# Performance work log

Hardware: AMD Instinct MI355X
Metric: run time of the kernel (lower is better)

## Reference

```python
import jax, jax.numpy as jnp
import numpy as np

B, L, D_MODEL = 2, 2048, 1024
HEADS, DH, K = 8, 128, 64  # d_head = d_model // heads, kernel_width window
DILATIONS = np.array([1, 1, 2, 2, 4, 4, 8, 8], dtype=np.int32)  # per-head dilation


def setup_inputs() -> dict:
    key = jax.random.key(0)
    ks = jax.random.split(key, 8)
    s_in = 1.0 / np.sqrt(D_MODEL)       # kaiming-uniform-ish fan_in bound
    s_c = 1.0 / np.sqrt(HEADS * DH)
    return {
        "query": jax.random.normal(ks[0], (B, L, D_MODEL), dtype=jnp.float32),
        "key": jax.random.normal(ks[1], (B, L, D_MODEL), dtype=jnp.float32),
        "value": jax.random.normal(ks[2], (B, L, D_MODEL), dtype=jnp.float32),
        "Wq": jax.random.uniform(ks[3], (HEADS, DH, D_MODEL), minval=-s_in, maxval=s_in),
        "bq": jnp.zeros((HEADS, DH), dtype=jnp.float32),
        "Wk": jax.random.uniform(ks[4], (HEADS, DH, D_MODEL), minval=-s_in, maxval=s_in),
        "bk": jnp.zeros((HEADS, DH), dtype=jnp.float32),
        "Wv": jax.random.uniform(ks[5], (HEADS, DH, D_MODEL), minval=-s_in, maxval=s_in),
        "bv": jnp.zeros((HEADS, DH), dtype=jnp.float32),
        "Wc": jax.random.uniform(ks[6], (D_MODEL, HEADS * DH), minval=-s_c, maxval=s_c),
        "bc": jnp.zeros((D_MODEL,), dtype=jnp.float32),
    }


def reference(query, key, value, Wq, bq, Wk, bk, Wv, bv, Wc, bc):
    Lq = query.shape[-2]
    # per-head linear projections: [B,L,D] x [H,DH,D] -> [B,H,L,DH]
    q = jnp.einsum('bld,hed->bhle', query, Wq) + bq[:, None, :]
    k = jnp.einsum('bld,hed->bhle', key, Wk) + bk[:, None, :]
    v = jnp.einsum('bld,hed->bhle', value, Wv) + bv[:, None, :]

    # dilated, centered local windows (per-head dilation)
    offsets = jnp.arange(K) - (K - 1) // 2                     # [K]
    dil = jnp.asarray(DILATIONS)                               # [H]
    idx = (jnp.arange(Lq)[None, :, None]
           + offsets[None, None, :] * dil[:, None, None])      # [H, L, K]
    valid = (idx >= 0) & (idx < Lq)
    idxc = jnp.clip(idx, 0, Lq - 1)

    # gather per-head windows: x [B,H,L,DH], idx [H,L,K] -> [B,H,L,K,DH]
    gather = jax.vmap(lambda xh, ih: xh[:, ih], in_axes=(1, 0), out_axes=1)
    k_win = gather(k, idxc)
    v_win = gather(v, idxc)

    # banded attention (original applies no 1/sqrt(d) scaling)
    scores = jnp.einsum('bhld,bhlkd->bhlk', q, k_win)
    scores = jnp.where(valid[None], scores, jnp.asarray(-1e9, scores.dtype))
    attn = jax.nn.softmax(scores, axis=-1)
    out = jnp.einsum('bhlk,bhlkd->bhld', attn, v_win)

    # merge heads and collapse back to d_model
    out = out.transpose(0, 2, 1, 3).reshape(out.shape[0], Lq, HEADS * DH)
    return out @ Wc.T + bc
```

## Files before the change

kernel.cpp:

```cpp
#include <hip/hip_runtime.h>
#include <hip/hip_bf16.h>
#include <stdint.h>

#define NB 2
#define LQ 2048
#define DMODEL 1024
#define NH 8
#define DH 128
#define KWIN 64

typedef __attribute__((ext_vector_type(8))) short short8;
typedef __attribute__((ext_vector_type(4))) float f32x4;

#define AS1 __attribute__((address_space(1)))
#define AS3 __attribute__((address_space(3)))

__device__ __forceinline__ ushort f2bf(float f) {
  uint u = __float_as_uint(f);
  return (ushort)((u + 0x7fffu + ((u >> 16) & 1u)) >> 16);
}
__device__ __forceinline__ float bflo(uint u) { return __uint_as_float(u << 16); }
__device__ __forceinline__ float bfhi(uint u) { return __uint_as_float(u & 0xffff0000u); }

__global__ void cvt_all(const float4* __restrict__ q, const float4* __restrict__ k,
                        const float4* __restrict__ v, const float4* __restrict__ wq,
                        const float4* __restrict__ wk, const float4* __restrict__ wv,
                        const float4* __restrict__ wc, ushort4* __restrict__ dst) {
  const int n4in = (NB * LQ * DMODEL) / 4;
  const int n4w = (NH * DH * DMODEL) / 4;
  const int total = 3 * n4in + 4 * n4w;
  const int stride = gridDim.x * blockDim.x;
  for (int i = blockIdx.x * blockDim.x + threadIdx.x; i < total; i += stride) {
    const float4* src;
    int off;
    if (i < 3 * n4in) {
      const int r = i >> 20;
      off = i & (n4in - 1);
      src = (r == 0) ? q : ((r == 1) ? k : v);
    } else {
      const int j = i - 3 * n4in;
      const int r = j >> 18;
      off = j & (n4w - 1);
      src = (r == 0) ? wq : ((r == 1) ? wk : ((r == 2) ? wv : wc));
    }
    float4 x = src[off];
    dst[i] = make_ushort4(f2bf(x.x), f2bf(x.y), f2bf(x.z), f2bf(x.w));
  }
}

__global__ __launch_bounds__(512, 2) void gemm256p(
    const ushort* __restrict__ A0, const ushort* __restrict__ B0,
    const float* __restrict__ c0, ushort* __restrict__ D0,
    const ushort* __restrict__ A1, const ushort* __restrict__ B1,
    const float* __restrict__ c1, ushort* __restrict__ D1,
    const ushort* __restrict__ A2, const ushort* __restrict__ B2,
    const float* __restrict__ c2, ushort* __restrict__ D2,
    int M, int N, int Kd) {
  const int gx = gridDim.x, gy = gridDim.y;
  const int nblk = gx * gy * gridDim.z;
  const int fid = (blockIdx.z * gy + blockIdx.y) * gx + blockIdx.x;
  const int cpx = nblk >> 3;
  const int nid = (fid & 7) * cpx + (fid >> 3);
  const int z = nid / (gx * gy);
  const int rem = nid % (gx * gy);
  const int m0 = (rem / gx) * 256;
  const int n0 = (rem % gx) * 256;

  const ushort* A = (z == 0) ? A0 : ((z == 1) ? A1 : A2);
  const ushort* Bt = (z == 0) ? B0 : ((z == 1) ? B1 : B2);
  const float* bias = (z == 0) ? c0 : ((z == 1) ? c1 : c2);
  ushort* Cv = (z == 0) ? D0 : ((z == 1) ? D1 : D2);

  __shared__ ushort LDS[4][16384];

  const int tid = threadIdx.x;
  const int wave = tid >> 6, lane = tid & 63;
  const int wm = wave >> 2, wn = wave & 3;
  const int lrow = lane & 15, kgrp = lane >> 4;

  const ushort* gsrc[4];
  int lofs[4];
#pragma unroll
  for (int qq = 0; qq < 4; ++qq) {
    const int half = qq & 1;
    const int o = half * 8192 + tid * 16;
    const int pr = o >> 7;
    const int s = (o >> 4) & 7;
    const int x = s ^ (pr & 7);
    const int row = 2 * pr + (x & 1);
    const int chunk = (x >> 1) * 8;
    lofs[qq] = (qq >> 1) * 8192 + half * 4096 + tid * 8;
    gsrc[qq] = (qq < 2) ? (A + (size_t)(m0 + row) * Kd + chunk)
                        : (Bt + (size_t)(n0 + row) * Kd + chunk);
  }

  auto STAGE2 = [&](int tt, int p) {
    ushort* sl = &LDS[tt & 3][0];
    const int kt = tt << 5;
    __builtin_amdgcn_global_load_lds((const AS1 void*)(gsrc[p] + kt),
                                     (AS3 void*)(sl + lofs[p]), 16, 0, 0);
    __builtin_amdgcn_global_load_lds((const AS1 void*)(gsrc[2 + p] + kt),
                                     (AS3 void*)(sl + lofs[2 + p]), 16, 0, 0);
  };

  int aoff[8], boff[4];
#pragma unroll
  for (int mi = 0; mi < 8; ++mi) {
    const int r = wm * 128 + mi * 16 + lrow;
    aoff[mi] = (r >> 1) * 64 + ((((kgrp << 1) | (r & 1)) ^ ((r >> 1) & 7)) * 8);
  }
#pragma unroll
  for (int ni = 0; ni < 4; ++ni) {
    const int r = wn * 64 + ni * 16 + lrow;
    boff[ni] = 8192 + (r >> 1) * 64 + ((((kgrp << 1) | (r & 1)) ^ ((r >> 1) & 7)) * 8);
  }

  f32x4 acc[8][4] = {};
  const int NT = Kd >> 5;

  STAGE2(0, 0); STAGE2(0, 1);
  STAGE2(1, 0); STAGE2(1, 1);

  for (int t = 0; t < NT; ++t) {
    const ushort* sl = &LDS[t & 3][0];
    if (t < NT - 2) {
      STAGE2(t + 2, 0);
      asm volatile("s_waitcnt vmcnt(6)" ::: "memory");
    } else if (t == NT - 2) {
      asm volatile("s_waitcnt vmcnt(4)" ::: "memory");
    } else {
      asm volatile("s_waitcnt vmcnt(0)" ::: "memory");
    }
    __builtin_amdgcn_sched_barrier(0);
    __builtin_amdgcn_s_barrier();
    __builtin_amdgcn_sched_barrier(0);

    short8 af[8], bfr[4];
#pragma unroll
    for (int m = 0; m < 4; ++m) af[m] = *(const short8*)(sl + aoff[m]);
#pragma unroll
    for (int n = 0; n < 4; ++n) bfr[n] = *(const short8*)(sl + boff[n]);
    asm volatile("s_waitcnt lgkmcnt(0)" ::: "memory");
    __builtin_amdgcn_sched_barrier(0);
    __builtin_amdgcn_s_setprio(1);
#pragma unroll
    for (int m = 0; m < 4; ++m)
#pragma unroll
      for (int n = 0; n < 4; ++n)
        acc[m][n] = __builtin_amdgcn_mfma_f32_16x16x32_bf16(af[m], bfr[n], acc[m][n], 0, 0, 0);
    __builtin_amdgcn_s_setprio(0);
    __builtin_amdgcn_sched_barrier(0);

    if (t < NT - 2) STAGE2(t + 2, 1);
#pragma unroll
    for (int m = 4; m < 8; ++m) af[m] = *(const short8*)(sl + aoff[m]);
    asm volatile("s_waitcnt lgkmcnt(0)" ::: "memory");
    __builtin_amdgcn_sched_barrier(0);
    __builtin_amdgcn_s_setprio(1);
#pragma unroll
    for (int m = 4; m < 8; ++m)
#pragma unroll
      for (int n = 0; n < 4; ++n)
        acc[m][n] = __builtin_amdgcn_mfma_f32_16x16x32_bf16(af[m], bfr[n], acc[m][n], 0, 0, 0);
    __builtin_amdgcn_s_setprio(0);
    __builtin_amdgcn_sched_barrier(0);
  }

  const int cbase = n0 + wn * 64;
  const int rbase = m0 + wm * 128;
  float bv[4];
#pragma unroll
  for (int n = 0; n < 4; ++n) bv[n] = bias[cbase + n * 16 + lrow];

#pragma unroll
  for (int m = 0; m < 8; ++m) {
#pragma unroll
    for (int n = 0; n < 4; ++n) {
      const int col = cbase + n * 16 + lrow;
#pragma unroll
      for (int j = 0; j < 4; ++j) {
        const int row = rbase + m * 16 + kgrp * 4 + j;
        Cv[(size_t)row * N + col] = f2bf(acc[m][n][j] + bv[n]);
      }
    }
  }
}

__global__ __launch_bounds__(256, 4) void gemm_out(
    const ushort* __restrict__ A, const ushort* __restrict__ Bt,
    const float* __restrict__ bias, float* __restrict__ Cv, int M, int N, int Kd) {
  const int gx = gridDim.x, gy = gridDim.y;
  const int nblk = gx * gy;
  const int fid = blockIdx.y * gx + blockIdx.x;
  const int cpx = nblk >> 3;
  const int nid = (fid & 7) * cpx + (fid >> 3);
  const int m0 = (nid / gx) * 128;
  const int n0 = (nid % gx) * 128;

  __shared__ ushort As[2][128 * 32];
  __shared__ ushort Bs[2][128 * 32];

  const int tid = threadIdx.x;
  const int wave = tid >> 6, lane = tid & 63;
  const int wm = wave >> 1, wn = wave & 1;
  const int lrow = lane & 15, kgrp = lane >> 4;

  const int b0 = tid * 16;
  const int b1 = b0 + 4096;
  const int r0 = b0 >> 6, cc0 = (b0 & 63) >> 1;
  const int r1 = b1 >> 6, cc1 = (b1 & 63) >> 1;

  const ushort* gA0 = A + (size_t)(m0 + r0) * Kd + cc0;
  const ushort* gA1 = A + (size_t)(m0 + r1) * Kd + cc1;
  const ushort* gB0 = Bt + (size_t)(n0 + r0) * Kd + cc0;
  const ushort* gB1 = Bt + (size_t)(n0 + r1) * Kd + cc1;

  auto stage = [&](int buf, int kt) {
    __builtin_amdgcn_global_load_lds((const AS1 void*)(gA0 + kt),
                                     (AS3 void*)(As[buf] + (b0 >> 1)), 16, 0, 0);
    __builtin_amdgcn_global_load_lds((const AS1 void*)(gA1 + kt),
                                     (AS3 void*)(As[buf] + (b1 >> 1)), 16, 0, 0);
    __builtin_amdgcn_global_load_lds((const AS1 void*)(gB0 + kt),
                                     (AS3 void*)(Bs[buf] + (b0 >> 1)), 16, 0, 0);
    __builtin_amdgcn_global_load_lds((const AS1 void*)(gB1 + kt),
                                     (AS3 void*)(Bs[buf] + (b1 >> 1)), 16, 0, 0);
  };

  f32x4 acc[4][4] = {};

  auto compute = [&](int buf) {
    short8 af[4], bfr[4];
#pragma unroll
    for (int m = 0; m < 4; ++m)
      af[m] = *(const short8*)(As[buf] + (wm * 64 + m * 16 + lrow) * 32 + kgrp * 8);
#pragma unroll
    for (int n = 0; n < 4; ++n)
      bfr[n] = *(const short8*)(Bs[buf] + (wn * 64 + n * 16 + lrow) * 32 + kgrp * 8);
#pragma unroll
    for (int m = 0; m < 4; ++m)
#pragma unroll
      for (int n = 0; n < 4; ++n)
        acc[m][n] = __builtin_amdgcn_mfma_f32_16x16x32_bf16(af[m], bfr[n], acc[m][n], 0, 0, 0);
  };

  const int nt = Kd >> 5;
  stage(0, 0);
  __syncthreads();
  int cur = 0;
  for (int it = 0; it < nt - 1; ++it) {
    stage(cur ^ 1, (it + 1) << 5);
    compute(cur);
    __syncthreads();
    cur ^= 1;
  }
  compute(cur);

  const int cbase = n0 + wn * 64;
  const int rbase = m0 + wm * 64;
  float bv[4];
#pragma unroll
  for (int n = 0; n < 4; ++n) bv[n] = bias[cbase + n * 16 + lrow];

#pragma unroll
  for (int m = 0; m < 4; ++m) {
#pragma unroll
    for (int n = 0; n < 4; ++n) {
      const int col = cbase + n * 16 + lrow;
#pragma unroll
      for (int j = 0; j < 4; ++j) {
        const int row = rbase + m * 16 + kgrp * 4 + j;
        Cv[(size_t)row * N + col] = acc[m][n][j] + bv[n];
      }
    }
  }
}

__global__ __launch_bounds__(128) void banded_attn_mfma(
    const ushort* __restrict__ qp, const ushort* __restrict__ kp,
    const ushort* __restrict__ vp, ushort* __restrict__ ao) {
  __shared__ ushort Qs[32 * 128];
  __shared__ ushort Ks[96 * 128];
  __shared__ ushort Vs[112 * 128];
  __shared__ ushort Ps[2][16 * 104];
  __shared__ ushort Os[2][16 * 128];

  const int tid = threadIdx.x;
  const int wv = tid >> 6;
  const int lane = tid & 63;
  const int lrow = lane & 15, kgrp = lane >> 4;

  const int blk = blockIdx.x;
  const int chunk = blk & 63;
  const int h = (blk >> 6) & 7;
  const int b = blk >> 9;
  const int sh = h >> 1;
  const int dil = 1 << sh;
  const int Ld = LQ >> sh;
  const int rres = chunk >> (6 - sh);
  const int tile = chunk & ((64 >> sh) - 1);
  const int t0 = tile << 5;
  const int p0 = t0 - 32;

  const size_t headoff = (size_t)h * DH;
  const size_t bbase = (size_t)b * LQ * (NH * DH);

  const int srow = lane >> 4;
  const int sc = lane & 15;
  for (int it = wv; it < 60; it += 2) {
    int rbase, pstart;
    const ushort* g;
    ushort* ld;
    if (it < 8) {
      rbase = it * 4; pstart = t0; g = qp; ld = Qs;
    } else if (it < 32) {
      rbase = (it - 8) * 4; pstart = p0; g = kp; ld = Ks;
    } else {
      rbase = (it - 32) * 4; pstart = p0; g = vp; ld = Vs;
    }
    int row = rbase + srow;
    int key = (row ^ (row >> 3)) & 7;
    int cs = sc ^ key;
    int t = pstart + row;
    t = t < 0 ? 0 : (t >= Ld ? Ld - 1 : t);
    int l = rres + t * dil;
    const ushort* src = g + bbase + (size_t)l * (NH * DH) + headoff + cs * 8;
    __builtin_amdgcn_global_load_lds((const AS1 void*)src,
                                     (AS3 void*)(ld + rbase * 128), 16, 0, 0);
  }
  __syncthreads();

  const int iblk = wv << 4;
  f32x4 accs[5] = {};
#pragma unroll
  for (int ks = 0; ks < 4; ++ks) {
    const int qrow = iblk + lrow;
    const int qslot = (ks * 4 + kgrp) ^ ((qrow ^ (qrow >> 3)) & 7);
    short8 qf = *(const short8*)(Qs + qrow * 128 + qslot * 8);
#pragma unroll
    for (int t = 0; t < 5; ++t) {
      const int krow = (wv + t) * 16 + lrow;
      const int kslot = (ks * 4 + kgrp) ^ ((krow ^ (krow >> 3)) & 7);
      short8 kf = *(const short8*)(Ks + krow * 128 + kslot * 8);
      accs[t] = __builtin_amdgcn_mfma_f32_16x16x32_bf16(qf, kf, accs[t], 0, 0, 0);
    }
  }

  float dens[4];
#pragma unroll
  for (int j = 0; j < 4; ++j) {
    const int i_b = iblk + kgrp * 4 + j;
    float mj = -1e30f;
#pragma unroll
    for (int t = 0; t < 5; ++t) {
      const int jj = (wv + t) * 16 + lrow;
      const int p = p0 + jj;
      const bool ok = (jj >= i_b + 1) && (jj <= i_b + 64) && (p >= 0) && (p < Ld);
      float v = ok ? accs[t][j] : -1e30f;
      accs[t][j] = v;
      mj = fmaxf(mj, v);
    }
#pragma unroll
    for (int off = 1; off < 16; off <<= 1) mj = fmaxf(mj, __shfl_xor(mj, off));
    float dj = 0.f;
#pragma unroll
    for (int t = 0; t < 5; ++t) {
      float e = __expf(accs[t][j] - mj);
      accs[t][j] = e;
      dj += e;
    }
#pragma unroll
    for (int off = 1; off < 16; off <<= 1) dj += __shfl_xor(dj, off);
    dens[j] = dj;
  }

  ushort* Pw = Ps[wv];
#pragma unroll
  for (int j = 0; j < 4; ++j) {
    const int prow = kgrp * 4 + j;
#pragma unroll
    for (int t = 0; t < 5; ++t) Pw[prow * 104 + t * 16 + lrow] = f2bf(accs[t][j]);
    Pw[prow * 104 + 80 + lrow] = 0;
  }

  f32x4 accv[8] = {};
#pragma unroll
  for (int ks = 0; ks < 3; ++ks) {
    short8 pf = *(const short8*)(Pw + lrow * 104 + ks * 32 + kgrp * 8);
#pragma unroll
    for (int dt = 0; dt < 8; ++dt) {
      short8 vf;
#pragma unroll
      for (int rr = 0; rr < 8; ++rr) {
        const int vrow = iblk + ks * 32 + kgrp * 8 + rr;
        const int d = dt * 16 + lrow;
        const int slot = (d >> 3) ^ ((vrow ^ (vrow >> 3)) & 7);
        vf[rr] = (short)Vs[vrow * 128 + slot * 8 + (d & 7)];
      }
      accv[dt] = __builtin_amdgcn_mfma_f32_16x16x32_bf16(pf, vf, accv[dt], 0, 0, 0);
    }
  }

  ushort* Ow = Os[wv];
#pragma unroll
  for (int j = 0; j < 4; ++j) {
    const float inv = 1.f / dens[j];
    const int orow = kgrp * 4 + j;
#pragma unroll
    for (int dt = 0; dt < 8; ++dt)
      Ow[orow * 128 + dt * 16 + lrow] = f2bf(accv[dt][j] * inv);
  }
#pragma unroll
  for (int pass = 0; pass < 4; ++pass) {
    const int i_loc = pass * 4 + srow;
    const int tq = t0 + iblk + i_loc;
    const int l = rres + tq * dil;
    short8 vvv = *(const short8*)(Ow + i_loc * 128 + sc * 8);
    *(short8*)(ao + bbase + (size_t)l * (NH * DH) + headoff + sc * 8) = vvv;
  }
}

extern "C" void kernel_launch(void* const* d_in, const int* in_sizes, int n_in,
                              void* d_out, int out_size, void* d_ws, size_t ws_size,
                              hipStream_t stream) {
  const float* q = (const float*)d_in[0];
  const float* k = (const float*)d_in[1];
  const float* v = (const float*)d_in[2];
  const float* Wq = (const float*)d_in[3];
  const float* bq = (const float*)d_in[4];
  const float* Wk = (const float*)d_in[5];
  const float* bk = (const float*)d_in[6];
  const float* Wv = (const float*)d_in[7];
  const float* bv = (const float*)d_in[8];
  const float* Wc = (const float*)d_in[9];
  const float* bc = (const float*)d_in[10];

  const size_t NIN = (size_t)NB * LQ * DMODEL;
  const size_t NW = (size_t)NH * DH * DMODEL;

  ushort* qin = (ushort*)d_ws;
  ushort* kin = qin + NIN;
  ushort* vin = kin + NIN;
  ushort* wqb = vin + NIN;
  ushort* wkb = wqb + NW;
  ushort* wvb = wkb + NW;
  ushort* wcb = wvb + NW;
  ushort* qp = wcb + NW;
  ushort* kp = qp + NIN;
  ushort* vp = kp + NIN;
  ushort* aob = vp + NIN;

  hipLaunchKernelGGL(cvt_all, dim3(2048), dim3(256), 0, stream,
                     (const float4*)q, (const float4*)k, (const float4*)v,
                     (const float4*)Wq, (const float4*)Wk, (const float4*)Wv,
                     (const float4*)Wc, (ushort4*)qin);

  dim3 g1(DMODEL / 256, (NB * LQ) / 256, 3);
  hipLaunchKernelGGL(gemm256p, g1, dim3(512), 0, stream,
                     qin, wqb, bq, qp,
                     kin, wkb, bk, kp,
                     vin, wvb, bv, vp,
                     NB * LQ, DMODEL, DMODEL);

  hipLaunchKernelGGL(banded_attn_mfma, dim3(NB * NH * 64), dim3(128), 0, stream,
                     qp, kp, vp, aob);

  dim3 g2(DMODEL / 128, (NB * LQ) / 128);
  hipLaunchKernelGGL(gemm_out, g2, dim3(256), 0, stream,
                     aob, wcb, bc, (float*)d_out, NB * LQ, DMODEL, DMODEL);
}
```

Measured before the change: 99.81 us.

## Fuse fp32-to-bf16 activation conversion into QKV projection GEMM loads

The separate conversion pass over the q/k/v activations is removed. The QKV GEMM now loads fp32 A tiles into registers, converts them to bf16 and writes them to LDS, while B tiles still go through direct global-to-LDS loads. The pipeline is reworked into a register-staged, three-deep prefetch with an unswizzled LDS layout, and the weight-only conversion kernel is simplified. This removes a full write and re-read of the bf16 activations. In exchange the GEMM reads twice as many A bytes, uses more registers, and the unswizzled LDS layout may cause bank conflicts.

```diff
diff --git a/kernel.cpp b/kernel.cpp
--- a/kernel.cpp
+++ b/kernel.cpp
@@ -22,38 +22,26 @@
 __device__ __forceinline__ float bflo(uint u) { return __uint_as_float(u << 16); }
 __device__ __forceinline__ float bfhi(uint u) { return __uint_as_float(u & 0xffff0000u); }
 
-__global__ void cvt_all(const float4* __restrict__ q, const float4* __restrict__ k,
-                        const float4* __restrict__ v, const float4* __restrict__ wq,
-                        const float4* __restrict__ wk, const float4* __restrict__ wv,
-                        const float4* __restrict__ wc, ushort4* __restrict__ dst) {
-  const int n4in = (NB * LQ * DMODEL) / 4;
-  const int n4w = (NH * DH * DMODEL) / 4;
-  const int total = 3 * n4in + 4 * n4w;
-  const int stride = gridDim.x * blockDim.x;
-  for (int i = blockIdx.x * blockDim.x + threadIdx.x; i < total; i += stride) {
-    const float4* src;
-    int off;
-    if (i < 3 * n4in) {
-      const int r = i >> 20;
-      off = i & (n4in - 1);
-      src = (r == 0) ? q : ((r == 1) ? k : v);
-    } else {
-      const int j = i - 3 * n4in;
-      const int r = j >> 18;
-      off = j & (n4w - 1);
-      src = (r == 0) ? wq : ((r == 1) ? wk : ((r == 2) ? wv : wc));
-    }
-    float4 x = src[off];
-    dst[i] = make_ushort4(f2bf(x.x), f2bf(x.y), f2bf(x.z), f2bf(x.w));
-  }
-}
-
-__global__ __launch_bounds__(512, 2) void gemm256p(
-    const ushort* __restrict__ A0, const ushort* __restrict__ B0,
+__global__ void cvt_w(const float4* __restrict__ a, const float4* __restrict__ b,
+                      const float4* __restrict__ c, const float4* __restrict__ d,
+                      ushort* __restrict__ da, ushort* __restrict__ db,
+                      ushort* __restrict__ dc, ushort* __restrict__ dd, int n4) {
+  int stride = gridDim.x * blockDim.x;
+  for (int i = blockIdx.x * blockDim.x + threadIdx.x; i < n4; i += stride) {
+    float4 x = a[i], y = b[i], z = c[i], w = d[i];
+    *(ushort4*)(da + 4 * (size_t)i) = make_ushort4(f2bf(x.x), f2bf(x.y), f2bf(x.z), f2bf(x.w));
+    *(ushort4*)(db + 4 * (size_t)i) = make_ushort4(f2bf(y.x), f2bf(y.y), f2bf(y.z), f2bf(y.w));
+    *(ushort4*)(dc + 4 * (size_t)i) = make_ushort4(f2bf(z.x), f2bf(z.y), f2bf(z.z), f2bf(z.w));
+    *(ushort4*)(dd + 4 * (size_t)i) = make_ushort4(f2bf(w.x), f2bf(w.y), f2bf(w.z), f2bf(w.w));
+  }
+}
+
+__global__ __launch_bounds__(512, 2) void gemm256f(
+    const float* __restrict__ A0f, const ushort* __restrict__ B0,
     const float* __restrict__ c0, ushort* __restrict__ D0,
-    const ushort* __restrict__ A1, const ushort* __restrict__ B1,
+    const float* __restrict__ A1f, const ushort* __restrict__ B1,
     const float* __restrict__ c1, ushort* __restrict__ D1,
-    const ushort* __restrict__ A2, const ushort* __restrict__ B2,
+    const float* __restrict__ A2f, const ushort* __restrict__ B2,
     const float* __restrict__ c2, ushort* __restrict__ D2,
     int M, int N, int Kd) {
   const int gx = gridDim.x, gy = gridDim.y;
@@ -66,7 +54,7 @@
   const int m0 = (rem / gx) * 256;
   const int n0 = (rem % gx) * 256;
 
-  const ushort* A = (z == 0) ? A0 : ((z == 1) ? A1 : A2);
+  const float* Af = (z == 0) ? A0f : ((z == 1) ? A1f : A2f);
   const ushort* Bt = (z == 0) ? B0 : ((z == 1) ? B1 : B2);
   const float* bias = (z == 0) ? c0 : ((z == 1) ? c1 : c2);
   ushort* Cv = (z == 0) ? D0 : ((z == 1) ? D1 : D2);
@@ -78,92 +66,103 @@
   const int wm = wave >> 2, wn = wave & 3;
   const int lrow = lane & 15, kgrp = lane >> 4;
 
-  const ushort* gsrc[4];
-  int lofs[4];
-#pragma unroll
-  for (int qq = 0; qq < 4; ++qq) {
-    const int half = qq & 1;
-    const int o = half * 8192 + tid * 16;
-    const int pr = o >> 7;
-    const int s = (o >> 4) & 7;
-    const int x = s ^ (pr & 7);
-    const int row = 2 * pr + (x & 1);
-    const int chunk = (x >> 1) * 8;
-    lofs[qq] = (qq >> 1) * 8192 + half * 4096 + tid * 8;
-    gsrc[qq] = (qq < 2) ? (A + (size_t)(m0 + row) * Kd + chunk)
-                        : (Bt + (size_t)(n0 + row) * Kd + chunk);
-  }
-
-  auto STAGE2 = [&](int tt, int p) {
+  const int ac0 = wave * 128 + lane;
+  const int ac1 = ac0 + 64;
+  const float* gA0 = Af + (size_t)(m0 + (ac0 >> 2)) * Kd + (ac0 & 3) * 8;
+  const float* gA1 = Af + (size_t)(m0 + (ac1 >> 2)) * Kd + (ac1 & 3) * 8;
+
+  const int o0 = tid * 16;
+  const int o1 = o0 + 8192;
+  const ushort* gB0 = Bt + (size_t)(n0 + (o0 >> 6)) * Kd + ((o0 & 63) >> 1);
+  const ushort* gB1 = Bt + (size_t)(n0 + (o1 >> 6)) * Kd + ((o1 & 63) >> 1);
+
+  float4 fa0[4], fa1[4];
+
+  auto AISSUE = [&](int tt, float4* d) {
+    const float* s0 = gA0 + (tt << 5);
+    const float* s1 = gA1 + (tt << 5);
+    d[0] = *(const float4*)(s0);
+    d[1] = *(const float4*)(s0 + 4);
+    d[2] = *(const float4*)(s1);
+    d[3] = *(const float4*)(s1 + 4);
+  };
+  auto BISSUE = [&](int tt) {
     ushort* sl = &LDS[tt & 3][0];
-    const int kt = tt << 5;
-    __builtin_amdgcn_global_load_lds((const AS1 void*)(gsrc[p] + kt),
-                                     (AS3 void*)(sl + lofs[p]), 16, 0, 0);
-    __builtin_amdgcn_global_load_lds((const AS1 void*)(gsrc[2 + p] + kt),
-                                     (AS3 void*)(sl + lofs[2 + p]), 16, 0, 0);
+    __builtin_amdgcn_global_load_lds((const AS1 void*)(gB0 + (tt << 5)),
+                                     (AS3 void*)(sl + 8192 + (o0 >> 1)), 16, 0, 0);
+    __builtin_amdgcn_global_load_lds((const AS1 void*)(gB1 + (tt << 5)),
+                                     (AS3 void*)(sl + 8192 + (o1 >> 1)), 16, 0, 0);
+  };
+  auto AWRITE = [&](int tt, const float4* d) {
+    ushort* sl = &LDS[tt & 3][0];
+    short8 w0, w1;
+    w0[0] = (short)f2bf(d[0].x); w0[1] = (short)f2bf(d[0].y);
+    w0[2] = (short)f2bf(d[0].z); w0[3] = (short)f2bf(d[0].w);
+    w0[4] = (short)f2bf(d[1].x); w0[5] = (short)f2bf(d[1].y);
+    w0[6] = (short)f2bf(d[1].z); w0[7] = (short)f2bf(d[1].w);
+    w1[0] = (short)f2bf(d[2].x); w1[1] = (short)f2bf(d[2].y);
+    w1[2] = (short)f2bf(d[2].z); w1[3] = (short)f2bf(d[2].w);
+    w1[4] = (short)f2bf(d[3].x); w1[5] = (short)f2bf(d[3].y);
+    w1[6] = (short)f2bf(d[3].z); w1[7] = (short)f2bf(d[3].w);
+    *(short8*)(sl + ac0 * 8) = w0;
+    *(short8*)(sl + ac1 * 8) = w1;
   };
 
   int aoff[8], boff[4];
 #pragma unroll
-  for (int mi = 0; mi < 8; ++mi) {
-    const int r = wm * 128 + mi * 16 + lrow;
-    aoff[mi] = (r >> 1) * 64 + ((((kgrp << 1) | (r & 1)) ^ ((r >> 1) & 7)) * 8);
-  }
-#pragma unroll
-  for (int ni = 0; ni < 4; ++ni) {
-    const int r = wn * 64 + ni * 16 + lrow;
-    boff[ni] = 8192 + (r >> 1) * 64 + ((((kgrp << 1) | (r & 1)) ^ ((r >> 1) & 7)) * 8);
-  }
+  for (int mi = 0; mi < 8; ++mi) aoff[mi] = (wm * 128 + mi * 16 + lrow) * 32 + kgrp * 8;
+#pragma unroll
+  for (int ni = 0; ni < 4; ++ni) boff[ni] = 8192 + (wn * 64 + ni * 16 + lrow) * 32 + kgrp * 8;
 
   f32x4 acc[8][4] = {};
   const int NT = Kd >> 5;
 
-  STAGE2(0, 0); STAGE2(0, 1);
-  STAGE2(1, 0); STAGE2(1, 1);
-
-  for (int t = 0; t < NT; ++t) {
+  AISSUE(0, fa0); BISSUE(0);
+  AISSUE(1, fa1); BISSUE(1);
+  asm volatile("s_waitcnt vmcnt(6)" ::: "memory");
+  __builtin_amdgcn_sched_barrier(0);
+  AWRITE(0, fa0);
+  AISSUE(2, fa0); BISSUE(2);
+  asm volatile("s_waitcnt lgkmcnt(0)" ::: "memory");
+  __builtin_amdgcn_sched_barrier(0);
+  __builtin_amdgcn_s_barrier();
+
+  auto BODY = [&](int t, float4* S) {
+    if (t < NT - 1) {
+      if (t < NT - 2) {
+        asm volatile("s_waitcnt vmcnt(6)" ::: "memory");
+      } else {
+        asm volatile("s_waitcnt vmcnt(0)" ::: "memory");
+      }
+      __builtin_amdgcn_sched_barrier(0);
+      AWRITE(t + 1, S);
+    }
+    if (t + 3 < NT) { AISSUE(t + 3, S); BISSUE(t + 3); }
+
     const ushort* sl = &LDS[t & 3][0];
-    if (t < NT - 2) {
-      STAGE2(t + 2, 0);
-      asm volatile("s_waitcnt vmcnt(6)" ::: "memory");
-    } else if (t == NT - 2) {
-      asm volatile("s_waitcnt vmcnt(4)" ::: "memory");
-    } else {
-      asm volatile("s_waitcnt vmcnt(0)" ::: "memory");
-    }
+    short8 af[8], bfr[4];
+#pragma unroll
+    for (int m = 0; m < 8; ++m) af[m] = *(const short8*)(sl + aoff[m]);
+#pragma unroll
+    for (int n = 0; n < 4; ++n) bfr[n] = *(const short8*)(sl + boff[n]);
+    asm volatile("s_waitcnt lgkmcnt(0)" ::: "memory");
     __builtin_amdgcn_sched_barrier(0);
     __builtin_amdgcn_s_barrier();
     __builtin_amdgcn_sched_barrier(0);
 
-    short8 af[8], bfr[4];
-#pragma unroll
-    for (int m = 0; m < 4; ++m) af[m] = *(const short8*)(sl + aoff[m]);
-#pragma unroll
-    for (int n = 0; n < 4; ++n) bfr[n] = *(const short8*)(sl + boff[n]);
-    asm volatile("s_waitcnt lgkmcnt(0)" ::: "memory");
-    __builtin_amdgcn_sched_barrier(0);
     __builtin_amdgcn_s_setprio(1);
 #pragma unroll
-    for (int m = 0; m < 4; ++m)
+    for (int m = 0; m < 8; ++m)
 #pragma unroll
       for (int n = 0; n < 4; ++n)
         acc[m][n] = __builtin_amdgcn_mfma_f32_16x16x32_bf16(af[m], bfr[n], acc[m][n], 0, 0, 0);
     __builtin_amdgcn_s_setprio(0);
     __builtin_amdgcn_sched_barrier(0);
-
-    if (t < NT - 2) STAGE2(t + 2, 1);
-#pragma unroll
-    for (int m = 4; m < 8; ++m) af[m] = *(const short8*)(sl + aoff[m]);
-    asm volatile("s_waitcnt lgkmcnt(0)" ::: "memory");
-    __builtin_amdgcn_sched_barrier(0);
-    __builtin_amdgcn_s_setprio(1);
-#pragma unroll
-    for (int m = 4; m < 8; ++m)
-#pragma unroll
-      for (int n = 0; n < 4; ++n)
-        acc[m][n] = __builtin_amdgcn_mfma_f32_16x16x32_bf16(af[m], bfr[n], acc[m][n], 0, 0, 0);
-    __builtin_amdgcn_s_setprio(0);
-    __builtin_amdgcn_sched_barrier(0);
+  };
+
+  for (int t = 0; t < NT; t += 2) {
+    BODY(t, fa1);
+    BODY(t + 1, fa0);
   }
 
   const int cbase = n0 + wn * 64;
@@ -437,10 +436,7 @@
   const size_t NIN = (size_t)NB * LQ * DMODEL;
   const size_t NW = (size_t)NH * DH * DMODEL;
 
-  ushort* qin = (ushort*)d_ws;
-  ushort* kin = qin + NIN;
-  ushort* vin = kin + NIN;
-  ushort* wqb = vin + NIN;
+  ushort* wqb = (ushort*)d_ws;
   ushort* wkb = wqb + NW;
   ushort* wvb = wkb + NW;
   ushort* wcb = wvb + NW;
@@ -449,16 +445,15 @@
   ushort* vp = kp + NIN;
   ushort* aob = vp + NIN;
 
-  hipLaunchKernelGGL(cvt_all, dim3(2048), dim3(256), 0, stream,
-                     (const float4*)q, (const float4*)k, (const float4*)v,
+  hipLaunchKernelGGL(cvt_w, dim3(1024), dim3(256), 0, stream,
                      (const float4*)Wq, (const float4*)Wk, (const float4*)Wv,
-                     (const float4*)Wc, (ushort4*)qin);
+                     (const float4*)Wc, wqb, wkb, wvb, wcb, (int)(NW / 4));
 
   dim3 g1(DMODEL / 256, (NB * LQ) / 256, 3);
-  hipLaunchKernelGGL(gemm256p, g1, dim3(512), 0, stream,
-                     qin, wqb, bq, qp,
-                     kin, wkb, bk, kp,
-                     vin, wvb, bv, vp,
+  hipLaunchKernelGGL(gemm256f, g1, dim3(512), 0, stream,
+                     q, wqb, bq, qp,
+                     k, wkb, bk, kp,
+                     v, wvb, bv, vp,
                      NB * LQ, DMODEL, DMODEL);
 
   hipLaunchKernelGGL(banded_attn_mfma, dim3(NB * NH * 64), dim3(128), 0, stream,
```

After: 101.4 us. About the same (+1.6%).

## Restructure QKV GEMM into 8-phase K=64 pipeline and shrink output GEMM tile

Applied to the files above, without the earlier changes.

Rewrites the fused QKV projection GEMM to use K-tiles of 64 with two LDS buffers split into quadrant halves. Each iteration runs eight phases that interleave LDS fragment reads, async global-to-LDS loads and MFMA quadrant blocks, with barriers between phases. The goal is to hide load latency behind matrix math more finely. The output GEMM tile drops from 128x128 to 128x64, doubling the block count to fill more CUs, at the cost of less reuse per block. The added barriers and the unswizzled B layout in the output GEMM may cost some throughput.

```diff
diff --git a/kernel.cpp b/kernel.cpp
--- a/kernel.cpp
+++ b/kernel.cpp
@@ -19,8 +19,6 @@
   uint u = __float_as_uint(f);
   return (ushort)((u + 0x7fffu + ((u >> 16) & 1u)) >> 16);
 }
-__device__ __forceinline__ float bflo(uint u) { return __uint_as_float(u << 16); }
-__device__ __forceinline__ float bfhi(uint u) { return __uint_as_float(u & 0xffff0000u); }
 
 __global__ void cvt_all(const float4* __restrict__ q, const float4* __restrict__ k,
                         const float4* __restrict__ v, const float4* __restrict__ wq,
@@ -48,199 +46,213 @@
   }
 }
 
-__global__ __launch_bounds__(512, 2) void gemm256p(
-    const ushort* __restrict__ A0, const ushort* __restrict__ B0,
+__global__ __launch_bounds__(512, 2) void gemm256_8p(
+    const ushort* __restrict__ A0p, const ushort* __restrict__ B0p,
     const float* __restrict__ c0, ushort* __restrict__ D0,
-    const ushort* __restrict__ A1, const ushort* __restrict__ B1,
+    const ushort* __restrict__ A1p, const ushort* __restrict__ B1p,
     const float* __restrict__ c1, ushort* __restrict__ D1,
-    const ushort* __restrict__ A2, const ushort* __restrict__ B2,
+    const ushort* __restrict__ A2p, const ushort* __restrict__ B2p,
     const float* __restrict__ c2, ushort* __restrict__ D2,
     int M, int N, int Kd) {
   const int gx = gridDim.x, gy = gridDim.y;
   const int nblk = gx * gy * gridDim.z;
   const int fid = (blockIdx.z * gy + blockIdx.y) * gx + blockIdx.x;
-  const int cpx = nblk >> 3;
-  const int nid = (fid & 7) * cpx + (fid >> 3);
+  const int nid = (fid & 7) * (nblk >> 3) + (fid >> 3);
   const int z = nid / (gx * gy);
   const int rem = nid % (gx * gy);
   const int m0 = (rem / gx) * 256;
   const int n0 = (rem % gx) * 256;
 
-  const ushort* A = (z == 0) ? A0 : ((z == 1) ? A1 : A2);
-  const ushort* Bt = (z == 0) ? B0 : ((z == 1) ? B1 : B2);
+  const ushort* A = (z == 0) ? A0p : ((z == 1) ? A1p : A2p);
+  const ushort* Bt = (z == 0) ? B0p : ((z == 1) ? B1p : B2p);
   const float* bias = (z == 0) ? c0 : ((z == 1) ? c1 : c2);
   ushort* Cv = (z == 0) ? D0 : ((z == 1) ? D1 : D2);
 
-  __shared__ ushort LDS[4][16384];
+  __shared__ ushort LDS[2][32768];
 
   const int tid = threadIdx.x;
   const int wave = tid >> 6, lane = tid & 63;
   const int wm = wave >> 2, wn = wave & 3;
   const int lrow = lane & 15, kgrp = lane >> 4;
 
-  const ushort* gsrc[4];
-  int lofs[4];
-#pragma unroll
-  for (int qq = 0; qq < 4; ++qq) {
-    const int half = qq & 1;
-    const int o = half * 8192 + tid * 16;
-    const int pr = o >> 7;
-    const int s = (o >> 4) & 7;
-    const int x = s ^ (pr & 7);
-    const int row = 2 * pr + (x & 1);
-    const int chunk = (x >> 1) * 8;
-    lofs[qq] = (qq >> 1) * 8192 + half * 4096 + tid * 8;
-    gsrc[qq] = (qq < 2) ? (A + (size_t)(m0 + row) * Kd + chunk)
-                        : (Bt + (size_t)(n0 + row) * Kd + chunk);
-  }
-
-  auto STAGE2 = [&](int tt, int p) {
-    ushort* sl = &LDS[tt & 3][0];
-    const int kt = tt << 5;
-    __builtin_amdgcn_global_load_lds((const AS1 void*)(gsrc[p] + kt),
-                                     (AS3 void*)(sl + lofs[p]), 16, 0, 0);
-    __builtin_amdgcn_global_load_lds((const AS1 void*)(gsrc[2 + p] + kt),
-                                     (AS3 void*)(sl + lofs[2 + p]), 16, 0, 0);
-  };
-
-  int aoff[8], boff[4];
-#pragma unroll
-  for (int mi = 0; mi < 8; ++mi) {
-    const int r = wm * 128 + mi * 16 + lrow;
-    aoff[mi] = (r >> 1) * 64 + ((((kgrp << 1) | (r & 1)) ^ ((r >> 1) & 7)) * 8);
-  }
-#pragma unroll
-  for (int ni = 0; ni < 4; ++ni) {
-    const int r = wn * 64 + ni * 16 + lrow;
-    boff[ni] = 8192 + (r >> 1) * 64 + ((((kgrp << 1) | (r & 1)) ^ ((r >> 1) & 7)) * 8);
-  }
-
+  int offA[2][2], offB[2][2];
+#pragma unroll
+  for (int u = 0; u < 2; ++u)
+#pragma unroll
+    for (int j = 0; j < 2; ++j) {
+      const int idx = j * 512 + tid;
+      const int s = idx >> 3, c = idx & 7;
+      const int cs = c ^ (s & 7);
+      const int rA = ((s >> 6) << 7) | (u << 6) | (s & 63);
+      const int rB = ((s >> 5) << 6) | (u << 5) | (s & 31);
+      offA[u][j] = (m0 + rA) * Kd + cs * 8;
+      offB[u][j] = (n0 + rB) * Kd + cs * 8;
+    }
+
+  auto STAGEA = [&](int bufb, int u, int T) {
+    ushort* dst = &LDS[bufb][u * 8192];
+#pragma unroll
+    for (int j = 0; j < 2; ++j)
+      __builtin_amdgcn_global_load_lds((const AS1 void*)(A + offA[u][j] + T * 64),
+                                       (AS3 void*)(dst + (j * 512 + tid) * 8), 16, 0, 0);
+  };
+  auto STAGEB = [&](int bufb, int u, int T) {
+    ushort* dst = &LDS[bufb][16384 + u * 8192];
+#pragma unroll
+    for (int j = 0; j < 2; ++j)
+      __builtin_amdgcn_global_load_lds((const AS1 void*)(Bt + offB[u][j] + T * 64),
+                                       (AS3 void*)(dst + (j * 512 + tid) * 8), 16, 0, 0);
+  };
+
+  const int sAb = (wm * 64 + lrow) * 64;
+  const int sBb = (wn * 32 + lrow) * 64;
+  int xk[2];
+#pragma unroll
+  for (int ks = 0; ks < 2; ++ks) xk[ks] = ((ks * 4 + kgrp) ^ (lrow & 7)) * 8;
+
+  short8 af[4][2], bf[2][2][2];
   f32x4 acc[8][4] = {};
-  const int NT = Kd >> 5;
-
-  STAGE2(0, 0); STAGE2(0, 1);
-  STAGE2(1, 0); STAGE2(1, 1);
-
-  for (int t = 0; t < NT; ++t) {
-    const ushort* sl = &LDS[t & 3][0];
-    if (t < NT - 2) {
-      STAGE2(t + 2, 0);
-      asm volatile("s_waitcnt vmcnt(6)" ::: "memory");
-    } else if (t == NT - 2) {
-      asm volatile("s_waitcnt vmcnt(4)" ::: "memory");
-    } else {
-      asm volatile("s_waitcnt vmcnt(0)" ::: "memory");
-    }
+
+  auto RDA = [&](int bufb, int mh) {
+#pragma unroll
+    for (int mi = 0; mi < 4; ++mi)
+#pragma unroll
+      for (int ks = 0; ks < 2; ++ks)
+        af[mi][ks] = *(const short8*)(&LDS[bufb][mh * 8192 + sAb + mi * 1024 + xk[ks]]);
+  };
+  auto RDB = [&](int bufb, int nh) {
+#pragma unroll
+    for (int ni = 0; ni < 2; ++ni)
+#pragma unroll
+      for (int ks = 0; ks < 2; ++ks)
+        bf[nh][ni][ks] =
+            *(const short8*)(&LDS[bufb][16384 + nh * 8192 + sBb + ni * 1024 + xk[ks]]);
+  };
+  auto MM = [&](int mh, int nh) {
+    __builtin_amdgcn_s_setprio(1);
+#pragma unroll
+    for (int mi = 0; mi < 4; ++mi)
+#pragma unroll
+      for (int ni = 0; ni < 2; ++ni)
+#pragma unroll
+        for (int ks = 0; ks < 2; ++ks)
+          acc[mh * 4 + mi][nh * 2 + ni] = __builtin_amdgcn_mfma_f32_16x16x32_bf16(
+              af[mi][ks], bf[nh][ni][ks], acc[mh * 4 + mi][nh * 2 + ni], 0, 0, 0);
+    __builtin_amdgcn_s_setprio(0);
+  };
+
+#define LGKM0()                                        \
+  asm volatile("s_waitcnt lgkmcnt(0)" ::: "memory");   \
+  __builtin_amdgcn_sched_barrier(0)
+#define BAR() __builtin_amdgcn_s_barrier()
+
+  const int NKT = Kd >> 6;
+  const int NIT = NKT >> 1;
+
+  STAGEA(0, 0, 0); STAGEB(0, 0, 0); STAGEA(0, 1, 0); STAGEB(0, 1, 0);
+  STAGEA(1, 0, 1); STAGEB(1, 0, 1);
+  asm volatile("s_waitcnt vmcnt(4)" ::: "memory");
+  __builtin_amdgcn_sched_barrier(0);
+  BAR();
+
+  for (int i = 0; i < NIT; ++i) {
+    const int ta = 2 * i, tb = ta + 1;
+    const bool sA = (ta + 2) < NKT, sB = (tb + 2) < NKT;
+    RDA(0, 0); RDB(0, 0);
+    STAGEA(1, 1, tb);
+    BAR(); LGKM0(); MM(0, 0); BAR();
+    RDB(0, 1);
+    STAGEB(1, 1, tb);
+    BAR(); LGKM0(); MM(0, 1); BAR();
+    RDA(0, 1);
+    if (sA) STAGEA(0, 0, ta + 2);
+    BAR(); LGKM0(); MM(1, 0); BAR();
+    if (sA) STAGEB(0, 0, ta + 2);
+    MM(1, 1);
+    if (sA) asm volatile("s_waitcnt vmcnt(4)" ::: "memory");
+    else    asm volatile("s_waitcnt vmcnt(0)" ::: "memory");
     __builtin_amdgcn_sched_barrier(0);
-    __builtin_amdgcn_s_barrier();
+    BAR();
+    RDA(1, 0); RDB(1, 0);
+    if (sA) STAGEA(0, 1, ta + 2);
+    BAR(); LGKM0(); MM(0, 0); BAR();
+    RDB(1, 1);
+    if (sA) STAGEB(0, 1, ta + 2);
+    BAR(); LGKM0(); MM(0, 1); BAR();
+    RDA(1, 1);
+    if (sB) STAGEA(1, 0, tb + 2);
+    BAR(); LGKM0(); MM(1, 0); BAR();
+    if (sB) STAGEB(1, 0, tb + 2);
+    MM(1, 1);
+    if (sB) asm volatile("s_waitcnt vmcnt(4)" ::: "memory");
+    else    asm volatile("s_waitcnt vmcnt(0)" ::: "memory");
     __builtin_amdgcn_sched_barrier(0);
-
-    short8 af[8], bfr[4];
-#pragma unroll
-    for (int m = 0; m < 4; ++m) af[m] = *(const short8*)(sl + aoff[m]);
-#pragma unroll
-    for (int n = 0; n < 4; ++n) bfr[n] = *(const short8*)(sl + boff[n]);
-    asm volatile("s_waitcnt lgkmcnt(0)" ::: "memory");
-    __builtin_amdgcn_sched_barrier(0);
-    __builtin_amdgcn_s_setprio(1);
-#pragma unroll
-    for (int m = 0; m < 4; ++m)
-#pragma unroll
-      for (int n = 0; n < 4; ++n)
-        acc[m][n] = __builtin_amdgcn_mfma_f32_16x16x32_bf16(af[m], bfr[n], acc[m][n], 0, 0, 0);
-    __builtin_amdgcn_s_setprio(0);
-    __builtin_amdgcn_sched_barrier(0);
-
-    if (t < NT - 2) STAGE2(t + 2, 1);
-#pragma unroll
-    for (int m = 4; m < 8; ++m) af[m] = *(const short8*)(sl + aoff[m]);
-    asm volatile("s_waitcnt lgkmcnt(0)" ::: "memory");
-    __builtin_amdgcn_sched_barrier(0);
-    __builtin_amdgcn_s_setprio(1);
-#pragma unroll
-    for (int m = 4; m < 8; ++m)
-#pragma unroll
-      for (int n = 0; n < 4; ++n)
-        acc[m][n] = __builtin_amdgcn_mfma_f32_16x16x32_bf16(af[m], bfr[n], acc[m][n], 0, 0, 0);
-    __builtin_amdgcn_s_setprio(0);
-    __builtin_amdgcn_sched_barrier(0);
-  }
+    BAR();
+  }
+#undef LGKM0
+#undef BAR
 
   const int cbase = n0 + wn * 64;
   const int rbase = m0 + wm * 128;
   float bv[4];
 #pragma unroll
   for (int n = 0; n < 4; ++n) bv[n] = bias[cbase + n * 16 + lrow];
-
-#pragma unroll
-  for (int m = 0; m < 8; ++m) {
+#pragma unroll
+  for (int m = 0; m < 8; ++m)
 #pragma unroll
     for (int n = 0; n < 4; ++n) {
       const int col = cbase + n * 16 + lrow;
 #pragma unroll
-      for (int j = 0; j < 4; ++j) {
-        const int row = rbase + m * 16 + kgrp * 4 + j;
-        Cv[(size_t)row * N + col] = f2bf(acc[m][n][j] + bv[n]);
-      }
-    }
-  }
-}
-
-__global__ __launch_bounds__(256, 4) void gemm_out(
+      for (int j = 0; j < 4; ++j)
+        Cv[(size_t)(rbase + m * 16 + kgrp * 4 + j) * N + col] = f2bf(acc[m][n][j] + bv[n]);
+    }
+}
+
+__global__ __launch_bounds__(256, 4) void gemm_out2(
     const ushort* __restrict__ A, const ushort* __restrict__ Bt,
     const float* __restrict__ bias, float* __restrict__ Cv, int M, int N, int Kd) {
-  const int gx = gridDim.x, gy = gridDim.y;
-  const int nblk = gx * gy;
+  const int gx = gridDim.x;
+  const int nblk = gx * gridDim.y;
   const int fid = blockIdx.y * gx + blockIdx.x;
-  const int cpx = nblk >> 3;
-  const int nid = (fid & 7) * cpx + (fid >> 3);
+  const int nid = (fid & 7) * (nblk >> 3) + (fid >> 3);
   const int m0 = (nid / gx) * 128;
-  const int n0 = (nid % gx) * 128;
+  const int n0 = (nid % gx) * 64;
 
   __shared__ ushort As[2][128 * 32];
-  __shared__ ushort Bs[2][128 * 32];
+  __shared__ ushort Bs[2][64 * 32];
 
   const int tid = threadIdx.x;
   const int wave = tid >> 6, lane = tid & 63;
-  const int wm = wave >> 1, wn = wave & 1;
+  const int wmO = wave >> 1, wnO = wave & 1;
   const int lrow = lane & 15, kgrp = lane >> 4;
 
-  const int b0 = tid * 16;
-  const int b1 = b0 + 4096;
-  const int r0 = b0 >> 6, cc0 = (b0 & 63) >> 1;
-  const int r1 = b1 >> 6, cc1 = (b1 & 63) >> 1;
-
-  const ushort* gA0 = A + (size_t)(m0 + r0) * Kd + cc0;
-  const ushort* gA1 = A + (size_t)(m0 + r1) * Kd + cc1;
-  const ushort* gB0 = Bt + (size_t)(n0 + r0) * Kd + cc0;
-  const ushort* gB1 = Bt + (size_t)(n0 + r1) * Kd + cc1;
+  const ushort* gA0 = A + (size_t)(m0 + (tid >> 2)) * Kd + (tid & 3) * 8;
+  const ushort* gA1 = A + (size_t)(m0 + 64 + (tid >> 2)) * Kd + (tid & 3) * 8;
+  const ushort* gB = Bt + (size_t)(n0 + (tid >> 2)) * Kd + (tid & 3) * 8;
 
   auto stage = [&](int buf, int kt) {
     __builtin_amdgcn_global_load_lds((const AS1 void*)(gA0 + kt),
-                                     (AS3 void*)(As[buf] + (b0 >> 1)), 16, 0, 0);
+                                     (AS3 void*)(As[buf] + tid * 8), 16, 0, 0);
     __builtin_amdgcn_global_load_lds((const AS1 void*)(gA1 + kt),
-                                     (AS3 void*)(As[buf] + (b1 >> 1)), 16, 0, 0);
-    __builtin_amdgcn_global_load_lds((const AS1 void*)(gB0 + kt),
-                                     (AS3 void*)(Bs[buf] + (b0 >> 1)), 16, 0, 0);
-    __builtin_amdgcn_global_load_lds((const AS1 void*)(gB1 + kt),
-                                     (AS3 void*)(Bs[buf] + (b1 >> 1)), 16, 0, 0);
-  };
-
-  f32x4 acc[4][4] = {};
-
+                                     (AS3 void*)(As[buf] + 2048 + tid * 8), 16, 0, 0);
+    __builtin_amdgcn_global_load_lds((const AS1 void*)(gB + kt),
+                                     (AS3 void*)(Bs[buf] + tid * 8), 16, 0, 0);
+  };
+
+  f32x4 acc[4][2] = {};
   auto compute = [&](int buf) {
-    short8 af[4], bfr[4];
-#pragma unroll
-    for (int m = 0; m < 4; ++m)
-      af[m] = *(const short8*)(As[buf] + (wm * 64 + m * 16 + lrow) * 32 + kgrp * 8);
-#pragma unroll
-    for (int n = 0; n < 4; ++n)
-      bfr[n] = *(const short8*)(Bs[buf] + (wn * 64 + n * 16 + lrow) * 32 + kgrp * 8);
-#pragma unroll
-    for (int m = 0; m < 4; ++m)
-#pragma unroll
-      for (int n = 0; n < 4; ++n)
-        acc[m][n] = __builtin_amdgcn_mfma_f32_16x16x32_bf16(af[m], bfr[n], acc[m][n], 0, 0, 0);
+    short8 af[4], bfr[2];
+#pragma unroll
+    for (int mi = 0; mi < 4; ++mi)
+      af[mi] = *(const short8*)(As[buf] + (wmO * 64 + mi * 16 + lrow) * 32 + kgrp * 8);
+#pragma unroll
+    for (int ni = 0; ni < 2; ++ni)
+      bfr[ni] = *(const short8*)(Bs[buf] + (wnO * 32 + ni * 16 + lrow) * 32 + kgrp * 8);
+#pragma unroll
+    for (int mi = 0; mi < 4; ++mi)
+#pragma unroll
+      for (int ni = 0; ni < 2; ++ni)
+        acc[mi][ni] = __builtin_amdgcn_mfma_f32_16x16x32_bf16(af[mi], bfr[ni], acc[mi][ni], 0, 0, 0);
   };
 
   const int nt = Kd >> 5;
@@ -255,24 +267,20 @@
   }
   compute(cur);
 
-  const int cbase = n0 + wn * 64;
-  const int rbase = m0 + wm * 64;
-  float bv[4];
-#pragma unroll
-  for (int n = 0; n < 4; ++n) bv[n] = bias[cbase + n * 16 + lrow];
-
-#pragma unroll
-  for (int m = 0; m < 4; ++m) {
-#pragma unroll
-    for (int n = 0; n < 4; ++n) {
-      const int col = cbase + n * 16 + lrow;
-#pragma unroll
-      for (int j = 0; j < 4; ++j) {
-        const int row = rbase + m * 16 + kgrp * 4 + j;
-        Cv[(size_t)row * N + col] = acc[m][n][j] + bv[n];
-      }
-    }
-  }
+  const int cbase = n0 + wnO * 32;
+  const int rbase = m0 + wmO * 64;
+  float bv[2];
+#pragma unroll
+  for (int ni = 0; ni < 2; ++ni) bv[ni] = bias[cbase + ni * 16 + lrow];
+#pragma unroll
+  for (int mi = 0; mi < 4; ++mi)
+#pragma unroll
+    for (int ni = 0; ni < 2; ++ni) {
+      const int col = cbase + ni * 16 + lrow;
+#pragma unroll
+      for (int j = 0; j < 4; ++j)
+        Cv[(size_t)(rbase + mi * 16 + kgrp * 4 + j) * N + col] = acc[mi][ni][j] + bv[ni];
+    }
 }
 
 __global__ __launch_bounds__(128) void banded_attn_mfma(
@@ -455,7 +463,7 @@
                      (const float4*)Wc, (ushort4*)qin);
 
   dim3 g1(DMODEL / 256, (NB * LQ) / 256, 3);
-  hipLaunchKernelGGL(gemm256p, g1, dim3(512), 0, stream,
+  hipLaunchKernelGGL(gemm256_8p, g1, dim3(512), 0, stream,
                      qin, wqb, bq, qp,
                      kin, wkb, bk, kp,
                      vin, wvb, bv, vp,
@@ -464,7 +472,7 @@
   hipLaunchKernelGGL(banded_attn_mfma, dim3(NB * NH * 64), dim3(128), 0, stream,
                      qp, kp, vp, aob);
 
-  dim3 g2(DMODEL / 128, (NB * LQ) / 128);
-  hipLaunchKernelGGL(gemm_out, g2, dim3(256), 0, stream,
+  dim3 g2(DMODEL / 64, (NB * LQ) / 128);
+  hipLaunchKernelGGL(gemm_out2, g2, dim3(256), 0, stream,
                      aob, wcb, bc, (float*)d_out, NB * LQ, DMODEL, DMODEL);
 }
```

Measured after the change: 94.55 us. -5.3%, faster.
